# Kernel tuning notes

Hardware: AMD Instinct MI355X
Metric: run time of the kernel (lower is better)

Reference implementation:

```python
import jax, jax.numpy as jnp
import numpy as np

B, S, D = 4, 4096, 1024

def setup_inputs() -> dict:
    key = jax.random.key(0)
    k1, k2 = jax.random.split(key)
    x = jax.random.normal(k1, (B, S, D), dtype=jnp.float32)
    W_qkv = jax.random.normal(k2, (D, 3 * D), dtype=jnp.float32) * (D ** -0.5)
    b_qkv = jnp.zeros((3 * D,), dtype=jnp.float32)
    return {"x": x, "W_qkv": W_qkv, "b_qkv": b_qkv}

def reference(x, W_qkv, b_qkv):
    # qkv projection: [B,S,3D]
    qkv = jnp.einsum('bsd,de->bse', x, W_qkv) + b_qkv
    q, k, v = jnp.split(qkv, 3, axis=-1)  # each [B,S,D]
    scale = q.shape[-1] ** -0.5
    # full [B,S,S] score matrix, as in the original (non-fused) implementation
    scores = jnp.einsum('bqd,bkd->bqk', q, k) * scale
    attn = jax.nn.softmax(scores, axis=-1)
    out = jnp.einsum('bqk,bkd->bqd', attn, v)
    return out
```

## Files before the change

### kernel.cpp

```cpp
#include <hip/hip_runtime.h>
#include <math.h>

typedef unsigned short ushort_t;
typedef __attribute__((ext_vector_type(8))) short short8;
typedef __attribute__((ext_vector_type(4))) float floatx4;

#define VMCNT(n) asm volatile("s_waitcnt vmcnt(" #n ")" ::: "memory")

__device__ inline ushort_t f2bf(float x) {
    union { float f; unsigned int u; } c; c.f = x;
    unsigned int r = (c.u + 0x7fffu + ((c.u >> 16) & 1u)) >> 16;
    return (ushort_t)r;
}

__device__ __forceinline__ void glds16(const ushort_t* g, ushort_t* l) {
    __builtin_amdgcn_global_load_lds(
        (const __attribute__((address_space(1))) unsigned int*)g,
        (__attribute__((address_space(3))) unsigned int*)l,
        16, 0, 0);
}

__device__ __forceinline__ unsigned swzo(unsigned off) {
    return off ^ ((off >> 3) & 0x70u);
}

__global__ __launch_bounds__(256)
void wt_kernel(const float* __restrict__ W, ushort_t* __restrict__ Wt)
{
    __shared__ float tile[64][65];
    const int k0 = blockIdx.x * 64;
    const int n0 = blockIdx.y * 64;
    const int tid = threadIdx.x;
    #pragma unroll
    for (int ii = 0; ii < 16; ++ii) {
        int idx = ii * 256 + tid;
        int r = idx >> 6, c = idx & 63;
        tile[r][c] = W[(size_t)(k0 + r) * 3072 + n0 + c];
    }
    __syncthreads();
    #pragma unroll
    for (int ii = 0; ii < 16; ++ii) {
        int idx = ii * 256 + tid;
        int r = idx >> 6, c = idx & 63;
        Wt[(size_t)(n0 + r) * 1024 + k0 + c] = f2bf(tile[c][r]);
    }
}

__global__ __launch_bounds__(256)
void xcvt(const float* __restrict__ x, ushort_t* __restrict__ xb)
{
    const int i = (blockIdx.x * 256 + threadIdx.x) * 8;
    float4 f0 = *(const float4*)(x + i);
    float4 f1 = *(const float4*)(x + i + 4);
    ushort_t tmp[8] __attribute__((aligned(16)));
    tmp[0]=f2bf(f0.x); tmp[1]=f2bf(f0.y); tmp[2]=f2bf(f0.z); tmp[3]=f2bf(f0.w);
    tmp[4]=f2bf(f1.x); tmp[5]=f2bf(f1.y); tmp[6]=f2bf(f1.z); tmp[7]=f2bf(f1.w);
    *(uint4*)(xb + i) = *(const uint4*)tmp;
}

__global__ __launch_bounds__(256)
void qkv_mfma(const float* __restrict__ x, const ushort_t* __restrict__ Wt,
              const float* __restrict__ bias,
              ushort_t* __restrict__ q, ushort_t* __restrict__ k,
              ushort_t* __restrict__ vt)
{
    __shared__ ushort_t As[128][72];
    __shared__ ushort_t Bs[128][72];
    const int tid = threadIdx.x;
    const int w = tid >> 6, lane = tid & 63;
    const int m = lane & 15, quad = lane >> 4;
    const int col0 = blockIdx.x * 128;
    const int r0   = blockIdx.y * 128;

    floatx4 o[2][8];
    #pragma unroll
    for (int rf = 0; rf < 2; ++rf)
        #pragma unroll
        for (int nf = 0; nf < 8; ++nf)
            o[rf][nf] = (floatx4){0.f, 0.f, 0.f, 0.f};

    for (int kc = 0; kc < 16; ++kc) {
        const int kdim = kc * 64;
        __syncthreads();
        #pragma unroll
        for (int ii = 0; ii < 4; ++ii) {
            int lin = ii * 256 + tid;
            int row = lin >> 3, seg = lin & 7;
            const float* src = x + (size_t)(r0 + row) * 1024 + kdim + seg * 8;
            float4 f0 = *(const float4*)src;
            float4 f1 = *(const float4*)(src + 4);
            ushort_t tmp[8] __attribute__((aligned(16)));
            tmp[0]=f2bf(f0.x); tmp[1]=f2bf(f0.y); tmp[2]=f2bf(f0.z); tmp[3]=f2bf(f0.w);
            tmp[4]=f2bf(f1.x); tmp[5]=f2bf(f1.y); tmp[6]=f2bf(f1.z); tmp[7]=f2bf(f1.w);
            *(uint4*)&As[row][seg * 8] = *(const uint4*)tmp;
        }
        #pragma unroll
        for (int ii = 0; ii < 4; ++ii) {
            int lin = ii * 256 + tid;
            int row = lin >> 3, seg = lin & 7;
            const ushort_t* src = Wt + (size_t)(col0 + row) * 1024 + kdim + seg * 8;
            *(uint4*)&Bs[row][seg * 8] = *(const uint4*)src;
        }
        __syncthreads();
        #pragma unroll
        for (int kk = 0; kk < 2; ++kk) {
            short8 af[2];
            #pragma unroll
            for (int rf = 0; rf < 2; ++rf)
                af[rf] = *(const short8*)&As[w * 32 + rf * 16 + m][kk * 32 + quad * 8];
            #pragma unroll
            for (int nf = 0; nf < 8; ++nf) {
                short8 bf = *(const short8*)&Bs[nf * 16 + m][kk * 32 + quad * 8];
                #pragma unroll
                for (int rf = 0; rf < 2; ++rf)
                    o[rf][nf] = __builtin_amdgcn_mfma_f32_16x16x32_bf16(af[rf], bf, o[rf][nf], 0, 0, 0);
            }
        }
    }

    const int which = col0 >> 10;
    const int dbase = col0 & 1023;
    float bias_v[8];
    #pragma unroll
    for (int nf = 0; nf < 8; ++nf) bias_v[nf] = bias[col0 + nf * 16 + m];

    #pragma unroll
    for (int rf = 0; rf < 2; ++rf) {
        #pragma unroll
        for (int e = 0; e < 4; ++e) {
            const int g = r0 + w * 32 + rf * 16 + quad * 4 + e;
            #pragma unroll
            for (int nf = 0; nf < 8; ++nf) {
                const int c = dbase + nf * 16 + m;
                float val = o[rf][nf][e] + bias_v[nf];
                if (which == 0) {
                    q[(size_t)g * 1024 + c] = f2bf(val * 0.03125f);
                } else if (which == 1) {
                    k[(size_t)g * 1024 + c] = f2bf(val);
                } else {
                    vt[(size_t)(g >> 12) * 4194304 + (size_t)c * 4096 + (g & 4095)] = f2bf(val);
                }
            }
        }
    }
}

__global__ __launch_bounds__(256)
void qkv_mfma2(const ushort_t* __restrict__ xb, const ushort_t* __restrict__ Wt,
               const float* __restrict__ bias,
               ushort_t* __restrict__ q, ushort_t* __restrict__ k,
               ushort_t* __restrict__ vt)
{
    __shared__ __align__(1024) ushort_t smem[2 * 128 * 64];
    ushort_t (*As)[64] = (ushort_t (*)[64])smem;
    ushort_t (*Bs)[64] = (ushort_t (*)[64])(smem + 128 * 64);
    const int tid = threadIdx.x;
    const int w = tid >> 6, lane = tid & 63;
    const int m = lane & 15, quad = lane >> 4;
    const int lx = lane ^ ((lane >> 3) & 7);
    const int sr = lx >> 3, sc = (lx & 7) * 8;
    const int col0 = blockIdx.x * 128;
    const int r0   = blockIdx.y * 128;

    floatx4 o[2][8];
    #pragma unroll
    for (int rf = 0; rf < 2; ++rf)
        #pragma unroll
        for (int nf = 0; nf < 8; ++nf)
            o[rf][nf] = (floatx4){0.f, 0.f, 0.f, 0.f};

    for (int kc = 0; kc < 16; ++kc) {
        const int kdim = kc * 64;
        __syncthreads();
        #pragma unroll
        for (int ii = 0; ii < 4; ++ii) {
            glds16(xb + (size_t)(r0 + w * 32 + ii * 8 + sr) * 1024 + kdim + sc,
                   &As[w * 32 + ii * 8][0]);
            glds16(Wt + (size_t)(col0 + w * 32 + ii * 8 + sr) * 1024 + kdim + sc,
                   &Bs[w * 32 + ii * 8][0]);
        }
        __syncthreads();
        #pragma unroll
        for (int kk = 0; kk < 2; ++kk) {
            short8 af[2];
            #pragma unroll
            for (int rf = 0; rf < 2; ++rf)
                af[rf] = *(const short8*)((const char*)As +
                          swzo((unsigned)((w * 32 + rf * 16 + m) * 128 + kk * 64 + quad * 16)));
            #pragma unroll
            for (int nf = 0; nf < 8; ++nf) {
                short8 bf = *(const short8*)((const char*)Bs +
                          swzo((unsigned)((nf * 16 + m) * 128 + kk * 64 + quad * 16)));
                #pragma unroll
                for (int rf = 0; rf < 2; ++rf)
                    o[rf][nf] = __builtin_amdgcn_mfma_f32_16x16x32_bf16(af[rf], bf, o[rf][nf], 0, 0, 0);
            }
        }
    }

    const int which = col0 >> 10;
    const int dbase = col0 & 1023;
    float bias_v[8];
    #pragma unroll
    for (int nf = 0; nf < 8; ++nf) bias_v[nf] = bias[col0 + nf * 16 + m];

    if (which == 2) {
        const size_t voffb = (size_t)(r0 >> 12) * 4194304;
        const int grow0 = r0 & 4095;
        ushort_t (*T)[136] = (ushort_t (*)[136])smem;
        #pragma unroll
        for (int p = 0; p < 2; ++p) {
            __syncthreads();
            #pragma unroll
            for (int rf = 0; rf < 2; ++rf)
                #pragma unroll
                for (int e = 0; e < 4; ++e) {
                    const int row = w * 32 + rf * 16 + quad * 4 + e;
                    #pragma unroll
                    for (int nn = 0; nn < 4; ++nn) {
                        const int nf = p * 4 + nn;
                        T[nn * 16 + m][row] = f2bf(o[rf][nf][e] + bias_v[nf]);
                    }
                }
            __syncthreads();
            #pragma unroll
            for (int ii = 0; ii < 4; ++ii) {
                int idx = ii * 256 + tid;
                int c = idx >> 4, seg = idx & 15;
                *(uint4*)&vt[voffb + (size_t)(dbase + p * 64 + c) * 4096 + grow0 + seg * 8]
                    = *(const uint4*)&T[c][seg * 8];
            }
        }
    } else {
        #pragma unroll
        for (int rf = 0; rf < 2; ++rf) {
            #pragma unroll
            for (int e = 0; e < 4; ++e) {
                const int g = r0 + w * 32 + rf * 16 + quad * 4 + e;
                #pragma unroll
                for (int nf = 0; nf < 8; ++nf) {
                    const int c = dbase + nf * 16 + m;
                    float val = o[rf][nf][e] + bias_v[nf];
                    if (which == 0) {
                        q[(size_t)g * 1024 + c] = f2bf(val * 0.03125f);
                    } else {
                        k[(size_t)g * 1024 + c] = f2bf(val);
                    }
                }
            }
        }
    }
}

__global__ __launch_bounds__(512, 2)
void fused_attn(const ushort_t* __restrict__ q, const ushort_t* __restrict__ kb_,
                const ushort_t* __restrict__ vt, float* __restrict__ out)
{
    __shared__ __align__(1024) unsigned char lds[141312];
    ushort_t (*Qs)[128][32] = (ushort_t(*)[128][32])(lds);
    ushort_t (*Ks)[256][32] = (ushort_t(*)[256][32])(lds + 24576);
    ushort_t (*Pls)[264]    = (ushort_t(*)[264])(lds);
    ushort_t (*Vs)[512][32] = (ushort_t(*)[512][32])(lds + 73728);
    float    (*redL)[4]     = (float(*)[4])(lds + 139264);

    const int tid  = threadIdx.x;
    const int w    = tid >> 6, lane = tid & 63;
    const int m    = lane & 15, quad = lane >> 4;
    const int wr   = w & 1, wc = w >> 1;
    const int lx   = lane ^ ((lane >> 3) & 7);
    const int lr   = lx >> 2, lc = (lx & 3) * 8;
    const int n0x  = blockIdx.x * 512;
    const int r0   = blockIdx.y * 128;
    const int b    = blockIdx.z;
    const size_t qoff = (size_t)b * 4096 * 1024;
    const size_t voff = (size_t)b * 4194304;

    unsigned qof[4], kof[4], vof[8];
    #pragma unroll
    for (int i = 0; i < 4; ++i)
        qof[i] = swzo((unsigned)((wr * 64 + i * 16 + m) * 64 + quad * 16));
    #pragma unroll
    for (int j = 0; j < 4; ++j)
        kof[j] = swzo((unsigned)((wc * 64 + j * 16 + m) * 64 + quad * 16));
    #pragma unroll
    for (int j = 0; j < 8; ++j)
        vof[j] = swzo((unsigned)((wc * 128 + j * 16 + m) * 64 + quad * 16));

    const ushort_t* qsrc  = q   + qoff + (size_t)(r0 + w * 16 + lr) * 1024 + lc;
    const ushort_t* ksrc0 = kb_ + qoff + (size_t)(w * 32 + lr) * 1024 + lc;
    const ushort_t* ksrc1 = kb_ + qoff + (size_t)(w * 32 + 16 + lr) * 1024 + lc;

    floatx4 o[4][8];
    #pragma unroll
    for (int i = 0; i < 4; ++i)
        #pragma unroll
        for (int j = 0; j < 8; ++j)
            o[i][j] = (floatx4){0.f, 0.f, 0.f, 0.f};
    float lsum[4][4] = {};

    for (int kt = 0; kt < 16; ++kt) {
        const int kbase = kt * 256;

        floatx4 s[4][4];
        #pragma unroll
        for (int i = 0; i < 4; ++i)
            #pragma unroll
            for (int j = 0; j < 4; ++j)
                s[i][j] = (floatx4){0.f, 0.f, 0.f, 0.f};

        glds16(qsrc,                        &Qs[0][w * 16][0]);
        glds16(ksrc0 + (size_t)kbase * 1024, &Ks[0][w * 32][0]);
        glds16(ksrc1 + (size_t)kbase * 1024, &Ks[0][w * 32 + 16][0]);
        {
            int cur = 0;
            for (int kc = 0; kc < 32; ++kc) {
                if (kc < 31) {
                    const int nxt = (cur == 2) ? 0 : cur + 1;
                    const int kd = (kc + 1) * 32;
                    glds16(qsrc + kd,                             &Qs[nxt][w * 16][0]);
                    glds16(ksrc0 + (size_t)kbase * 1024 + kd,     &Ks[nxt][w * 32][0]);
                    glds16(ksrc1 + (size_t)kbase * 1024 + kd,     &Ks[nxt][w * 32 + 16][0]);
                    VMCNT(3);
                } else {
                    VMCNT(0);
                }
                __builtin_amdgcn_s_barrier();
                __builtin_amdgcn_sched_barrier(0);
                short8 af[4], bf[4];
                #pragma unroll
                for (int i = 0; i < 4; ++i)
                    af[i] = *(const short8*)((const char*)Qs[cur] + qof[i]);
                #pragma unroll
                for (int j = 0; j < 4; ++j)
                    bf[j] = *(const short8*)((const char*)Ks[cur] + kof[j]);
                __builtin_amdgcn_s_setprio(1);
                #pragma unroll
                for (int i = 0; i < 4; ++i)
                    #pragma unroll
                    for (int j = 0; j < 4; ++j)
                        s[i][j] = __builtin_amdgcn_mfma_f32_16x16x32_bf16(af[i], bf[j], s[i][j], 0, 0, 0);
                __builtin_amdgcn_s_setprio(0);
                cur = (cur == 2) ? 0 : cur + 1;
            }
        }
        __syncthreads();

        #pragma unroll
        for (int i = 0; i < 4; ++i)
            glds16(vt + voff + (size_t)(n0x + w * 64 + i * 16 + lr) * 4096 + kbase + lc,
                   &Vs[0][w * 64 + i * 16][0]);

        #pragma unroll
        for (int i = 0; i < 4; ++i)
            #pragma unroll
            for (int j = 0; j < 4; ++j)
                #pragma unroll
                for (int e = 0; e < 4; ++e) {
                    float pv = __expf(s[i][j][e]);
                    lsum[i][e] += pv;
                    Pls[wr * 64 + i * 16 + quad * 4 + e][wc * 64 + j * 16 + m] = f2bf(pv);
                }
        __syncthreads();

        for (int vc = 0; vc < 8; ++vc) {
            const int p = vc & 1;
            if (vc < 7) {
                const int kd = kbase + (vc + 1) * 32;
                #pragma unroll
                for (int i = 0; i < 4; ++i)
                    glds16(vt + voff + (size_t)(n0x + w * 64 + i * 16 + lr) * 4096 + kd + lc,
                           &Vs[p ^ 1][w * 64 + i * 16][0]);
            }
            short8 ap[4], bv[8];
            #pragma unroll
            for (int i = 0; i < 4; ++i)
                ap[i] = *(const short8*)&Pls[wr * 64 + i * 16 + m][vc * 32 + quad * 8];
            #pragma unroll
            for (int j = 0; j < 8; ++j)
                bv[j] = *(const short8*)((const char*)Vs[p] + vof[j]);
            __builtin_amdgcn_s_setprio(1);
            #pragma unroll
            for (int i = 0; i < 4; ++i)
                #pragma unroll
                for (int j = 0; j < 8; ++j)
                    o[i][j] = __builtin_amdgcn_mfma_f32_16x16x32_bf16(ap[i], bv[j], o[i][j], 0, 0, 0);
            __builtin_amdgcn_s_setprio(0);
            __syncthreads();
        }
    }

    #pragma unroll
    for (int i = 0; i < 4; ++i)
        #pragma unroll
        for (int e = 0; e < 4; ++e) {
            float l = lsum[i][e];
            l += __shfl_xor(l, 1);
            l += __shfl_xor(l, 2);
            l += __shfl_xor(l, 4);
            l += __shfl_xor(l, 8);
            if (m == 0) redL[wr * 64 + i * 16 + quad * 4 + e][wc] = l;
        }
    __syncthreads();
    #pragma unroll
    for (int i = 0; i < 4; ++i)
        #pragma unroll
        for (int e = 0; e < 4; ++e) {
            const int row = wr * 64 + i * 16 + quad * 4 + e;
            const float inv = 1.0f / (redL[row][0] + redL[row][1] + redL[row][2] + redL[row][3]);
            const int g = b * 4096 + r0 + row;
            #pragma unroll
            for (int j = 0; j < 8; ++j)
                out[(size_t)g * 1024 + n0x + wc * 128 + j * 16 + m] = o[i][j][e] * inv;
        }
}

extern "C" void kernel_launch(void* const* d_in, const int* in_sizes, int n_in,
                              void* d_out, int out_size, void* d_ws, size_t ws_size,
                              hipStream_t stream)
{
    const float* x    = (const float*)d_in[0];
    const float* W    = (const float*)d_in[1];
    const float* bias = (const float*)d_in[2];
    float* out = (float*)d_out;

    const size_t SZQ  = (size_t)4 * 4096 * 1024 * 2;
    const size_t SZWT = (size_t)3072 * 1024 * 2;
    const size_t SZXB = (size_t)4 * 4096 * 1024 * 2;
    const size_t NEED  = 3 * SZQ + SZWT;
    const size_t NEED2 = NEED + SZXB;
    if (ws_size < NEED) return;

    ushort_t* q  = (ushort_t*)d_ws;
    ushort_t* k  = (ushort_t*)((char*)d_ws + SZQ);
    ushort_t* vt = (ushort_t*)((char*)d_ws + 2 * SZQ);
    ushort_t* Wt = (ushort_t*)((char*)d_ws + 3 * SZQ);
    ushort_t* xb = (ushort_t*)((char*)d_ws + NEED);

    wt_kernel <<<dim3(16, 48),   256, 0, stream>>>(W, Wt);
    if (ws_size >= NEED2) {
        xcvt      <<<dim3(8192),    256, 0, stream>>>(x, xb);
        qkv_mfma2 <<<dim3(24, 128), 256, 0, stream>>>(xb, Wt, bias, q, k, vt);
    } else {
        qkv_mfma  <<<dim3(24, 128), 256, 0, stream>>>(x, Wt, bias, q, k, vt);
    }
    fused_attn<<<dim3(2, 32, 4), 512, 0, stream>>>(q, k, vt, out);
}
```

Measured before the change: 744.7 us.

## Transpose QK MFMA operands for vectorized P stores and remap block grid

Swaps the A/B operands of the QK^T MFMA so each lane holds four consecutive key columns for one query row. The probabilities can then be packed into one 8-byte LDS store instead of four scalar 2-byte stores. The row-sum reduction shrinks to two cross-quad shuffles. The launch becomes a 1D grid with a custom block-to-(batch, column-half, row-tile) mapping, intended to improve K/V cache sharing across XCDs, and the V prefetch now issues after the exp stage.

Result: faster. 688.0 us (-7.6%).

```diff
diff --git a/kernel.cpp b/kernel.cpp
--- a/kernel.cpp
+++ b/kernel.cpp
@@ -269,9 +269,11 @@
     const int wr   = w & 1, wc = w >> 1;
     const int lx   = lane ^ ((lane >> 3) & 7);
     const int lr   = lx >> 2, lc = (lx & 3) * 8;
-    const int n0x  = blockIdx.x * 512;
-    const int r0   = blockIdx.y * 128;
-    const int b    = blockIdx.z;
+    const int bid  = blockIdx.x;
+    const int b    = (bid & 7) >> 1;
+    const int n    = ((bid >> 3) << 1) | (bid & 1);
+    const int n0x  = (n >> 5) * 512;
+    const int r0   = (n & 31) * 128;
     const size_t qoff = (size_t)b * 4096 * 1024;
     const size_t voff = (size_t)b * 4194304;
 
@@ -296,17 +298,17 @@
         #pragma unroll
         for (int j = 0; j < 8; ++j)
             o[i][j] = (floatx4){0.f, 0.f, 0.f, 0.f};
-    float lsum[4][4] = {};
+    float lsum[4] = {};
 
     for (int kt = 0; kt < 16; ++kt) {
         const int kbase = kt * 256;
 
         floatx4 s[4][4];
         #pragma unroll
-        for (int i = 0; i < 4; ++i)
-            #pragma unroll
-            for (int j = 0; j < 4; ++j)
-                s[i][j] = (floatx4){0.f, 0.f, 0.f, 0.f};
+        for (int j = 0; j < 4; ++j)
+            #pragma unroll
+            for (int i = 0; i < 4; ++i)
+                s[j][i] = (floatx4){0.f, 0.f, 0.f, 0.f};
 
         glds16(qsrc,                        &Qs[0][w * 16][0]);
         glds16(ksrc0 + (size_t)kbase * 1024, &Ks[0][w * 32][0]);
@@ -335,10 +337,10 @@
                     bf[j] = *(const short8*)((const char*)Ks[cur] + kof[j]);
                 __builtin_amdgcn_s_setprio(1);
                 #pragma unroll
-                for (int i = 0; i < 4; ++i)
+                for (int j = 0; j < 4; ++j)
                     #pragma unroll
-                    for (int j = 0; j < 4; ++j)
-                        s[i][j] = __builtin_amdgcn_mfma_f32_16x16x32_bf16(af[i], bf[j], s[i][j], 0, 0, 0);
+                    for (int i = 0; i < 4; ++i)
+                        s[j][i] = __builtin_amdgcn_mfma_f32_16x16x32_bf16(bf[j], af[i], s[j][i], 0, 0, 0);
                 __builtin_amdgcn_s_setprio(0);
                 cur = (cur == 2) ? 0 : cur + 1;
             }
@@ -347,19 +349,25 @@
 
         #pragma unroll
         for (int i = 0; i < 4; ++i)
-            glds16(vt + voff + (size_t)(n0x + w * 64 + i * 16 + lr) * 4096 + kbase + lc,
-                   &Vs[0][w * 64 + i * 16][0]);
-
-        #pragma unroll
-        for (int i = 0; i < 4; ++i)
-            #pragma unroll
-            for (int j = 0; j < 4; ++j)
-                #pragma unroll
-                for (int e = 0; e < 4; ++e) {
-                    float pv = __expf(s[i][j][e]);
-                    lsum[i][e] += pv;
-                    Pls[wr * 64 + i * 16 + quad * 4 + e][wc * 64 + j * 16 + m] = f2bf(pv);
-                }
+            #pragma unroll
+            for (int j = 0; j < 4; ++j) {
+                float p0 = __expf(s[j][i][0]);
+                float p1 = __expf(s[j][i][1]);
+                float p2 = __expf(s[j][i][2]);
+                float p3 = __expf(s[j][i][3]);
+                lsum[i] += (p0 + p1) + (p2 + p3);
+                unsigned lo = (unsigned)f2bf(p0) | ((unsigned)f2bf(p1) << 16);
+                unsigned hi = (unsigned)f2bf(p2) | ((unsigned)f2bf(p3) << 16);
+                *(uint2*)&Pls[wr * 64 + i * 16 + m][wc * 64 + j * 16 + quad * 4] =
+                    (uint2){lo, hi};
+            }
+
+        {
+            #pragma unroll
+            for (int i = 0; i < 4; ++i)
+                glds16(vt + voff + (size_t)(n0x + w * 64 + i * 16 + lr) * 4096 + kbase + lc,
+                       &Vs[0][w * 64 + i * 16][0]);
+        }
         __syncthreads();
 
         for (int vc = 0; vc < 8; ++vc) {
@@ -390,16 +398,12 @@
     }
 
     #pragma unroll
-    for (int i = 0; i < 4; ++i)
-        #pragma unroll
-        for (int e = 0; e < 4; ++e) {
-            float l = lsum[i][e];
-            l += __shfl_xor(l, 1);
-            l += __shfl_xor(l, 2);
-            l += __shfl_xor(l, 4);
-            l += __shfl_xor(l, 8);
-            if (m == 0) redL[wr * 64 + i * 16 + quad * 4 + e][wc] = l;
-        }
+    for (int i = 0; i < 4; ++i) {
+        float l = lsum[i];
+        l += __shfl_xor(l, 16);
+        l += __shfl_xor(l, 32);
+        if (quad == 0) redL[wr * 64 + i * 16 + m][wc] = l;
+    }
     __syncthreads();
     #pragma unroll
     for (int i = 0; i < 4; ++i)
@@ -443,5 +447,5 @@
     } else {
         qkv_mfma  <<<dim3(24, 128), 256, 0, stream>>>(x, Wt, bias, q, k, vt);
     }
-    fused_attn<<<dim3(2, 32, 4), 512, 0, stream>>>(q, k, vt, out);
-}
+    fused_attn<<<dim3(256), 512, 0, stream>>>(q, k, vt, out);
+}
```
